# Optimization experiments

Hardware: AMD Instinct MI355X
Metric: run time of the kernel (lower is better)

## Reference

```python
import jax, jax.numpy as jnp
import numpy as np

N = 4096      # atoms
K = 5         # atoms gathered per cell (top_k in put_atoms_in_cells)
M = 8         # neighbors kept per atom
NBR = 26      # neighbor cells per cell (9+9+8)

def _grid():
    # get_cells: box [-10,10) step 1 Angstrom -> 20^3 = 8000 cells
    g = jnp.arange(-10.0, 10.0, 1.0)
    X = jnp.stack(jnp.meshgrid(g, g, g))       # (3,20,20,20), tf.meshgrid default 'xy'
    return jnp.transpose(X).reshape(-1, 3)      # (8000,3)

def _sqdist(a, b):
    # ||a_i - b_j||^2 via expansion; avoids (A,B,3) intermediate
    return (jnp.sum(a * a, 1)[:, None] + jnp.sum(b * b, 1)[None, :] - 2.0 * (a @ b.T))

def _neighbor_list(coords):
    cells = _grid()                              # (n_cells, 3)
    # put_atoms_in_cells: tf.nn.top_k(norm, k) -> k LARGEST norms (faithful to source)
    d_ca = _sqdist(cells, coords)                # (n_cells, N)
    _, atoms_in_cells = jax.lax.top_k(d_ca, K)   # (n_cells, K)
    # get_cells_for_atoms: top_k(-norm, 1) -> closest cell per atom
    d_ac = _sqdist(coords, cells)                # (N, n_cells)
    cells_for_atoms = jnp.argmin(d_ac, axis=1)   # (N,)
    # compute_neighbor_cells: top_k(norm, 26) (faithful to source)
    d_cc = _sqdist(cells, cells)                 # (n_cells, n_cells)
    _, nbr_cells = jax.lax.top_k(d_cc, NBR)      # (n_cells, 26)
    nbr_cells_atom = nbr_cells[cells_for_atoms]  # (N, 26)
    nbr_inds = atoms_in_cells[nbr_cells_atom]    # (N, 26, K)
    nbr_coords = coords[nbr_inds]                # (N, 26, K, 3)
    dists = jnp.sum((coords[:, None, None, :] - nbr_coords) ** 2, axis=-1)
    dists = dists.reshape(N, NBR * K)            # (N, 130)
    _, locs = jax.lax.top_k(dists, M)            # top_k(dists, M) as in source
    flat = nbr_inds.reshape(N, NBR * K)
    return jnp.take_along_axis(flat, locs, axis=1)   # (N, M) atom indices

def _energy(coords, vdw, weights, nrot, nbr):
    # d_ij = r_ij - R_i - R_j
    diff = coords[:, None, :] - coords[nbr]      # (N, M, 3)
    r = jnp.sqrt(jnp.sum(diff * diff, axis=-1) + 1e-12)
    d = r - vdw[:, None] - vdw[nbr]
    g1 = jnp.exp(-(d / 0.5) ** 2)
    g2 = jnp.exp(-((d - 3.0) / 2.0) ** 2)
    rep = jnp.where(d < 0.0, d * d, 0.0)
    hyd = jnp.where(d < 0.5, 1.0, jnp.where(d < 1.5, 1.5 - d, 0.0))
    hb = jnp.where(d < -0.7, 1.0, jnp.where(d < 0.0, -d / 0.7, 0.0))
    hval = (weights[0] * g1 + weights[1] * g2 + weights[2] * rep
            + weights[3] * hyd + weights[4] * hb)
    f = jnp.where(d < 8.0, hval, 0.0)            # cutoff at 8 Angstrom
    c = jnp.sum(f)
    return c / (1.0 + weights[5] * nrot[0])      # g(c, Nrot)

def setup_inputs() -> dict:
    key = jax.random.key(0)
    k1, k2, k3 = jax.random.split(key, 3)
    coords = jax.random.uniform(k1, (N, 3), jnp.float32, -10.0, 10.0)
    vdw = jax.random.uniform(k2, (N,), jnp.float32, 1.0, 2.0)
    weights = 0.3 * jax.random.normal(k3, (6,), jnp.float32)
    nrot = 8.0 * jnp.ones((1,), jnp.float32)
    return {"coords": coords, "vdw": vdw, "weights": weights, "nrot": nrot}

def reference(coords, vdw, weights, nrot):
    nbr = _neighbor_list(coords)
    return _energy(coords, vdw, weights, nrot, nbr)
```

## Files before the change

kernel.cpp:

```cpp
#include <hip/hip_runtime.h>
#include <stdint.h>

#define NATOMS 4096
#define NCELLS 8000
#define KTOP 5
#define MNBR 8
#define NBRC 26
#define HBINS 217
#define LSTMAX 512

__device__ __forceinline__ unsigned long long umax64(unsigned long long a, unsigned long long b) {
    return a > b ? a : b;
}
__device__ __forceinline__ unsigned long long umin64(unsigned long long a, unsigned long long b) {
    return a < b ? a : b;
}

__device__ __forceinline__ void cell_coords_i(int m, int& x, int& y, int& z) {
    int a = m / 400;
    int r = m - a * 400;
    int b = r / 20;
    int c = r - b * 20;
    x = b - 10; y = c - 10; z = a - 10;
}

__global__ __launch_bounds__(256) void k1_cells_nbr(const float* __restrict__ coords,
                                                    int* __restrict__ cellsForAtoms,
                                                    int* __restrict__ nbrTable,
                                                    int* __restrict__ neededFlag) {
    const int atom = blockIdx.x;
    const int t = threadIdx.x;
    const int lane = t & 63;

    __shared__ int sCi;
    __shared__ uint32_t h[HBINS];
    __shared__ int lst[LSTMAX];
    __shared__ int sV, cnt;

    if (t < HBINS) h[t] = 0;
    if (t == 0) cnt = 0;

    if (t < 64) {
        float ax = coords[atom * 3], ay = coords[atom * 3 + 1], az = coords[atom * 3 + 2];
        float sa = __fadd_rn(__fadd_rn(__fmul_rn(ax, ax), __fmul_rn(ay, ay)), __fmul_rn(az, az));

        int fx = (int)floorf(ax), fy = (int)floorf(ay), fz = (int)floorf(az);
        int vx = min(9, max(-10, fx - 1 + (lane & 3)));
        int vy = min(9, max(-10, fy - 1 + ((lane >> 2) & 3)));
        int vz = min(9, max(-10, fz - 1 + (lane >> 4)));
        int m = (vz + 10) * 400 + (vx + 10) * 20 + (vy + 10);

        float cx = (float)vx, cy = (float)vy, cz = (float)vz;
        float scell = (float)(vx * vx + vy * vy + vz * vz);
        float dot = __fadd_rn(__fadd_rn(__fmul_rn(ax, cx), __fmul_rn(ay, cy)), __fmul_rn(az, cz));
        float val = __fsub_rn(__fadd_rn(sa, scell), __fmul_rn(2.0f, dot));
        unsigned long long key = ((unsigned long long)__float_as_uint(val) << 32) | (unsigned int)m;

        for (int off = 32; off > 0; off >>= 1)
            key = umin64(key, (unsigned long long)__shfl_xor((long long)key, off));
        if (lane == 0) {
            int c = (int)(key & 0xFFFFFFFFull);
            cellsForAtoms[atom] = c;
            sCi = c;
        }
    }
    __syncthreads();

    const int ci = sCi;
    int xi, yi, zi;
    cell_coords_i(ci, xi, yi, zi);
    const int Lx = max(xi + 10, 9 - xi);
    const int Ly = max(yi + 10, 9 - yi);
    const int Lz = max(zi + 10, 9 - zi);

    int lo;
    {
        int px[3] = { Lx * Lx, (Lx - 1) * (Lx - 1), (Lx - 2) * (Lx - 2) };
        int py[3] = { Ly * Ly, (Ly - 1) * (Ly - 1), (Ly - 2) * (Ly - 2) };
        int pz[3] = { Lz * Lz, (Lz - 1) * (Lz - 1), (Lz - 2) * (Lz - 2) };
        int m1 = 0x7FFFFFFF, m2 = 0x7FFFFFFF;
#pragma unroll
        for (int a = 0; a < 3; ++a)
#pragma unroll
            for (int b = 0; b < 3; ++b)
#pragma unroll
                for (int c = 0; c < 3; ++c) {
                    int s = px[a] + py[b] + pz[c];
                    if (s < m1) { m2 = m1; m1 = s; }
                    else if (s < m2) m2 = s;
                }
        lo = m2;
    }

#pragma unroll
    for (int col = 0; col < 2; ++col) {
        int p = t + 256 * col;
        if (p < 400) {
            int bb = p / 20, cc = p - bb * 20;
            int dxv = xi - (bb - 10), dyv = yi - (cc - 10);
            int Dbc = dxv * dxv + dyv * dyv;
            int R = lo - Dbc;
            int aLoEnd = 19, aHiStart = 20;
            if (R > 0) {
                int t0 = (int)ceilf(sqrtf((float)R));
                if ((t0 - 1) * (t0 - 1) >= R) --t0;
                if (t0 * t0 < R) ++t0;
                aLoEnd = min(19, zi + 10 - t0);
                aHiStart = max(0, zi + 10 + t0);
            }
            for (int a = 0; a <= aLoEnd; ++a) {
                int dzv = zi - (a - 10);
                atomicAdd(&h[Dbc + dzv * dzv - lo], 1u);
            }
            for (int a = aHiStart; a < 20; ++a) {
                int dzv = zi - (a - 10);
                atomicAdd(&h[Dbc + dzv * dzv - lo], 1u);
            }
        }
    }
    __syncthreads();

    if (t < 64) {
        int c4[4];
        int cnt4 = 0;
#pragma unroll
        for (int k = 0; k < 4; ++k) {
            int b = (HBINS - 1) - (t * 4 + k);
            c4[k] = (b >= 0) ? (int)h[b] : 0;
            cnt4 += c4[k];
        }
        int incl = cnt4;
        for (int off = 1; off < 64; off <<= 1) {
            int v = __shfl_up(incl, off);
            if (lane >= off) incl += v;
        }
        int P = incl - cnt4;
        if (P < NBRC && incl >= NBRC) {
            int run = P;
#pragma unroll
            for (int k = 0; k < 4; ++k) {
                run += c4[k];
                if (run >= NBRC) { sV = lo + (HBINS - 1) - (t * 4 + k); break; }
            }
        }
    }
    __syncthreads();
    const int V = sV;

#pragma unroll
    for (int col = 0; col < 2; ++col) {
        int p = t + 256 * col;
        if (p < 400) {
            int bb = p / 20, cc = p - bb * 20;
            int dxv = xi - (bb - 10), dyv = yi - (cc - 10);
            int Dbc = dxv * dxv + dyv * dyv;
            int R = V - Dbc;
            int aLoEnd = 19, aHiStart = 20;
            if (R > 0) {
                int t0 = (int)ceilf(sqrtf((float)R));
                if ((t0 - 1) * (t0 - 1) >= R) --t0;
                if (t0 * t0 < R) ++t0;
                aLoEnd = min(19, zi + 10 - t0);
                aHiStart = max(0, zi + 10 + t0);
            }
            for (int a = 0; a <= aLoEnd; ++a) {
                int dzv = zi - (a - 10);
                int d = Dbc + dzv * dzv;
                int j = a * 400 + p;
                int q = atomicAdd(&cnt, 1);
                if (q < LSTMAX) lst[q] = (d << 13) | (8191 - j);
            }
            for (int a = aHiStart; a < 20; ++a) {
                int dzv = zi - (a - 10);
                int d = Dbc + dzv * dzv;
                int j = a * 400 + p;
                int q = atomicAdd(&cnt, 1);
                if (q < LSTMAX) lst[q] = (d << 13) | (8191 - j);
            }
        }
    }
    __syncthreads();

    int n = min(cnt, LSTMAX);
    if (t < 64) {
        for (int base = 0; base < n; base += 64) {
            int idx = base + t;
            int key = (idx < n) ? lst[idx] : -1;
            int rank = 0;
            for (int m = 0; m < n; ++m) rank += (lst[m] > key) ? 1 : 0;
            if (idx < n && rank < NBRC) {
                int j = 8191 - (key & 8191);
                nbrTable[ci * NBRC + rank] = j;
                neededFlag[j] = 1;
            }
        }
    }
}

__global__ __launch_bounds__(256) void k2_atoms(const float* __restrict__ coords,
                                                const int* __restrict__ neededFlag,
                                                int* __restrict__ atomsInCells) {
    const int i = blockIdx.x;
    if (neededFlag[i] != 1) return;
    __shared__ unsigned long long redB[4];
    const int t = threadIdx.x;
    const int lane = t & 63, wv = t >> 6;

    int xi_, yi_, zi_;
    cell_coords_i(i, xi_, yi_, zi_);
    const float cx = (float)xi_, cy = (float)yi_, cz = (float)zi_;
    const float scell = (float)(xi_ * xi_ + yi_ * yi_ + zi_ * zi_);

    unsigned long long keys[16];
#pragma unroll
    for (int s = 0; s < 16; ++s) {
        int j = t + 256 * s;
        float ax = coords[j * 3], ay = coords[j * 3 + 1], az = coords[j * 3 + 2];
        float sa = __fadd_rn(__fadd_rn(__fmul_rn(ax, ax), __fmul_rn(ay, ay)), __fmul_rn(az, az));
        float dot = __fadd_rn(__fadd_rn(__fmul_rn(cx, ax), __fmul_rn(cy, ay)), __fmul_rn(cz, az));
        float val = __fsub_rn(__fadd_rn(scell, sa), __fmul_rn(2.0f, dot));
        keys[s] = ((unsigned long long)__float_as_uint(val) << 32) | (unsigned int)(4095 - j);
    }

    for (int r = 0; r < KTOP; ++r) {
        unsigned long long best = 0ull;
#pragma unroll
        for (int s = 0; s < 16; ++s) best = umax64(best, keys[s]);
        for (int off = 32; off > 0; off >>= 1)
            best = umax64(best, (unsigned long long)__shfl_xor((long long)best, off));
        if (lane == 0) redB[wv] = best;
        __syncthreads();
        unsigned long long wbest = umax64(umax64(redB[0], redB[1]), umax64(redB[2], redB[3]));
        if (t == 0) atomsInCells[i * KTOP + r] = 4095 - (int)(wbest & 0xFFFFFFFFull);
#pragma unroll
        for (int s = 0; s < 16; ++s) if (keys[s] == wbest) keys[s] = 0ull;
        __syncthreads();
    }
}

__global__ __launch_bounds__(256) void k3_energy(const float* __restrict__ coords,
                                                 const float* __restrict__ vdw,
                                                 const float* __restrict__ weights,
                                                 const int* __restrict__ nbrTable,
                                                 const int* __restrict__ atomsInCells,
                                                 const int* __restrict__ cellsForAtoms,
                                                 float* __restrict__ partials) {
    const int wid = threadIdx.x >> 6;
    const int lane = threadIdx.x & 63;
    const int i = blockIdx.x * 4 + wid;

    const float xi = coords[i * 3], yi = coords[i * 3 + 1], zi = coords[i * 3 + 2];
    const int ci = cellsForAtoms[i];

    int cand[3];
    unsigned long long keys[3];
#pragma unroll
    for (int s = 0; s < 3; ++s) {
        int p = lane + 64 * s;
        cand[s] = -1;
        keys[s] = 0ull;
        if (p < NBRC * KTOP) {
            int cellSlot = p / KTOP;
            int atomSlot = p - cellSlot * KTOP;
            int nc = nbrTable[ci * NBRC + cellSlot];
            int j = atomsInCells[nc * KTOP + atomSlot];
            cand[s] = j;
            float dx = __fsub_rn(xi, coords[j * 3]);
            float dy = __fsub_rn(yi, coords[j * 3 + 1]);
            float dz = __fsub_rn(zi, coords[j * 3 + 2]);
            float dist = __fadd_rn(__fadd_rn(__fmul_rn(dx, dx), __fmul_rn(dy, dy)), __fmul_rn(dz, dz));
            keys[s] = ((unsigned long long)__float_as_uint(dist) << 8) | (unsigned int)(255 - p);
        }
    }

    const float w0 = weights[0], w1 = weights[1], w2 = weights[2];
    const float w3 = weights[3], w4 = weights[4];
    const float vi = vdw[i];

    float esum = 0.0f;
    for (int r = 0; r < MNBR; ++r) {
        unsigned long long best = umax64(umax64(keys[0], keys[1]), keys[2]);
        for (int off = 32; off > 0; off >>= 1)
            best = umax64(best, (unsigned long long)__shfl_xor((long long)best, off));

        int p = 255 - (int)(best & 0xFFull);
        int slot = p >> 6;
        int owner = p & 63;
        int jsel = (slot == 0) ? cand[0] : (slot == 1) ? cand[1] : cand[2];
        int j = __shfl(jsel, owner);
        float dist = __uint_as_float((unsigned int)(best >> 8));

#pragma unroll
        for (int s = 0; s < 3; ++s) if (keys[s] == best) keys[s] = 0ull;

        float rr = __fsqrt_rn(__fadd_rn(dist, 1e-12f));
        float d = __fsub_rn(__fsub_rn(rr, vi), vdw[j]);
        float t1 = __fdiv_rn(d, 0.5f);
        float g1 = expf(-__fmul_rn(t1, t1));
        float t2 = __fdiv_rn(__fsub_rn(d, 3.0f), 2.0f);
        float g2 = expf(-__fmul_rn(t2, t2));
        float rep = (d < 0.0f) ? __fmul_rn(d, d) : 0.0f;
        float hyd = (d < 0.5f) ? 1.0f : ((d < 1.5f) ? __fsub_rn(1.5f, d) : 0.0f);
        float hb = (d < -0.7f) ? 1.0f : ((d < 0.0f) ? __fdiv_rn(-d, 0.7f) : 0.0f);
        float hval = __fadd_rn(__fadd_rn(__fadd_rn(__fadd_rn(
                         __fmul_rn(w0, g1), __fmul_rn(w1, g2)),
                         __fmul_rn(w2, rep)), __fmul_rn(w3, hyd)), __fmul_rn(w4, hb));
        float f = (d < 8.0f) ? hval : 0.0f;
        esum = __fadd_rn(esum, f);
    }
    if (lane == 0) partials[i] = esum;
}

__global__ __launch_bounds__(256) void k4_reduce(const float* __restrict__ partials,
                                                 const float* __restrict__ weights,
                                                 const float* __restrict__ nrot,
                                                 float* __restrict__ out) {
    __shared__ float red[256];
    const int t = threadIdx.x;
    float s = 0.0f;
    for (int k = 0; k < NATOMS / 256; ++k) s = __fadd_rn(s, partials[t + 256 * k]);
    red[t] = s;
    __syncthreads();
    for (int off = 128; off > 0; off >>= 1) {
        if (t < off) red[t] = __fadd_rn(red[t], red[t + off]);
        __syncthreads();
    }
    if (t == 0) out[0] = __fdiv_rn(red[0], __fadd_rn(1.0f, __fmul_rn(weights[5], nrot[0])));
}

extern "C" void kernel_launch(void* const* d_in, const int* in_sizes, int n_in,
                              void* d_out, int out_size, void* d_ws, size_t ws_size,
                              hipStream_t stream) {
    const float* coords  = (const float*)d_in[0];
    const float* vdw     = (const float*)d_in[1];
    const float* weights = (const float*)d_in[2];
    const float* nrot    = (const float*)d_in[3];
    float* out = (float*)d_out;

    int* nbrTable      = (int*)d_ws;
    int* atomsInCells  = nbrTable + NCELLS * NBRC;
    int* cellsForAtoms = atomsInCells + NCELLS * KTOP;
    int* neededFlag    = cellsForAtoms + NATOMS;
    float* partials    = (float*)(neededFlag + NCELLS);

    k1_cells_nbr<<<NATOMS, 256, 0, stream>>>(coords, cellsForAtoms, nbrTable, neededFlag);
    k2_atoms<<<NCELLS, 256, 0, stream>>>(coords, neededFlag, atomsInCells);
    k3_energy<<<NATOMS / 4, 256, 0, stream>>>(coords, vdw, weights, nbrTable,
                                              atomsInCells, cellsForAtoms, partials);
    k4_reduce<<<1, 256, 0, stream>>>(partials, weights, nrot, out);
}
```

Measured before the change: 42.56 us.

## Simplify farthest-cell enumeration, per-wave top-k merge, and cache atom norms

The 27-way threshold search in the neighbor-cell kernel becomes a closed-form lower bound, and the sqrt-based z-range computation becomes early-break scans from both ends of the z column. Ranking of the candidate list now spreads over all 256 threads instead of one wave. In the atom-gather kernel, each wave keeps its own top-5 with no per-round block barriers, and a final rank-merge of 20 candidates picks the block's top-5. Atom squared norms computed in the first kernel are reused in the second to avoid recomputation. The risks are subtle correctness changes in the lower bound and in ties during the wave merge.

Result: faster. 39.49 us (-7.2%).

```diff
diff --git a/kernel.cpp b/kernel.cpp
--- a/kernel.cpp
+++ b/kernel.cpp
@@ -6,7 +6,7 @@
 #define KTOP 5
 #define MNBR 8
 #define NBRC 26
-#define HBINS 217
+#define HBINS 184
 #define LSTMAX 512
 
 __device__ __forceinline__ unsigned long long umax64(unsigned long long a, unsigned long long b) {
@@ -26,6 +26,7 @@
 
 __global__ __launch_bounds__(256) void k1_cells_nbr(const float* __restrict__ coords,
                                                     int* __restrict__ cellsForAtoms,
+                                                    float* __restrict__ sumsq,
                                                     int* __restrict__ nbrTable,
                                                     int* __restrict__ neededFlag) {
     const int atom = blockIdx.x;
@@ -61,6 +62,7 @@
         if (lane == 0) {
             int c = (int)(key & 0xFFFFFFFFull);
             cellsForAtoms[atom] = c;
+            sumsq[atom] = sa;
             sCi = c;
         }
     }
@@ -72,25 +74,9 @@
     const int Lx = max(xi + 10, 9 - xi);
     const int Ly = max(yi + 10, 9 - yi);
     const int Lz = max(zi + 10, 9 - zi);
-
-    int lo;
-    {
-        int px[3] = { Lx * Lx, (Lx - 1) * (Lx - 1), (Lx - 2) * (Lx - 2) };
-        int py[3] = { Ly * Ly, (Ly - 1) * (Ly - 1), (Ly - 2) * (Ly - 2) };
-        int pz[3] = { Lz * Lz, (Lz - 1) * (Lz - 1), (Lz - 2) * (Lz - 2) };
-        int m1 = 0x7FFFFFFF, m2 = 0x7FFFFFFF;
-#pragma unroll
-        for (int a = 0; a < 3; ++a)
-#pragma unroll
-            for (int b = 0; b < 3; ++b)
-#pragma unroll
-                for (int c = 0; c < 3; ++c) {
-                    int s = px[a] + py[b] + pz[c];
-                    if (s < m1) { m2 = m1; m1 = s; }
-                    else if (s < m2) m2 = s;
-                }
-        lo = m2;
-    }
+    const int lo = (Lx - 2) * (Lx - 2) + (Ly - 2) * (Ly - 2) + (Lz - 2) * (Lz - 2)
+                 + 2 * min(Lx, min(Ly, Lz)) - 3;
+    const int A0 = zi + 10;
 
 #pragma unroll
     for (int col = 0; col < 2; ++col) {
@@ -99,22 +85,20 @@
             int bb = p / 20, cc = p - bb * 20;
             int dxv = xi - (bb - 10), dyv = yi - (cc - 10);
             int Dbc = dxv * dxv + dyv * dyv;
-            int R = lo - Dbc;
-            int aLoEnd = 19, aHiStart = 20;
-            if (R > 0) {
-                int t0 = (int)ceilf(sqrtf((float)R));
-                if ((t0 - 1) * (t0 - 1) >= R) --t0;
-                if (t0 * t0 < R) ++t0;
-                aLoEnd = min(19, zi + 10 - t0);
-                aHiStart = max(0, zi + 10 + t0);
-            }
-            for (int a = 0; a <= aLoEnd; ++a) {
-                int dzv = zi - (a - 10);
-                atomicAdd(&h[Dbc + dzv * dzv - lo], 1u);
-            }
-            for (int a = aHiStart; a < 20; ++a) {
-                int dzv = zi - (a - 10);
-                atomicAdd(&h[Dbc + dzv * dzv - lo], 1u);
+            int a = 0;
+            for (; a < 20; ++a) {
+                int dz = A0 - a;
+                int d = Dbc + dz * dz;
+                if (d < lo) break;
+                atomicAdd(&h[d - lo], 1u);
+            }
+            if (a < 20) {
+                for (int a2 = 19; a2 >= a; --a2) {
+                    int dz = A0 - a2;
+                    int d = Dbc + dz * dz;
+                    if (d < lo) break;
+                    atomicAdd(&h[d - lo], 1u);
+                }
             }
         }
     }
@@ -154,55 +138,47 @@
             int bb = p / 20, cc = p - bb * 20;
             int dxv = xi - (bb - 10), dyv = yi - (cc - 10);
             int Dbc = dxv * dxv + dyv * dyv;
-            int R = V - Dbc;
-            int aLoEnd = 19, aHiStart = 20;
-            if (R > 0) {
-                int t0 = (int)ceilf(sqrtf((float)R));
-                if ((t0 - 1) * (t0 - 1) >= R) --t0;
-                if (t0 * t0 < R) ++t0;
-                aLoEnd = min(19, zi + 10 - t0);
-                aHiStart = max(0, zi + 10 + t0);
-            }
-            for (int a = 0; a <= aLoEnd; ++a) {
-                int dzv = zi - (a - 10);
-                int d = Dbc + dzv * dzv;
-                int j = a * 400 + p;
+            int a = 0;
+            for (; a < 20; ++a) {
+                int dz = A0 - a;
+                int d = Dbc + dz * dz;
+                if (d < V) break;
                 int q = atomicAdd(&cnt, 1);
-                if (q < LSTMAX) lst[q] = (d << 13) | (8191 - j);
-            }
-            for (int a = aHiStart; a < 20; ++a) {
-                int dzv = zi - (a - 10);
-                int d = Dbc + dzv * dzv;
-                int j = a * 400 + p;
-                int q = atomicAdd(&cnt, 1);
-                if (q < LSTMAX) lst[q] = (d << 13) | (8191 - j);
+                if (q < LSTMAX) lst[q] = (d << 13) | (8191 - (a * 400 + p));
+            }
+            if (a < 20) {
+                for (int a2 = 19; a2 >= a; --a2) {
+                    int dz = A0 - a2;
+                    int d = Dbc + dz * dz;
+                    if (d < V) break;
+                    int q = atomicAdd(&cnt, 1);
+                    if (q < LSTMAX) lst[q] = (d << 13) | (8191 - (a2 * 400 + p));
+                }
             }
         }
     }
     __syncthreads();
 
     int n = min(cnt, LSTMAX);
-    if (t < 64) {
-        for (int base = 0; base < n; base += 64) {
-            int idx = base + t;
-            int key = (idx < n) ? lst[idx] : -1;
-            int rank = 0;
-            for (int m = 0; m < n; ++m) rank += (lst[m] > key) ? 1 : 0;
-            if (idx < n && rank < NBRC) {
-                int j = 8191 - (key & 8191);
-                nbrTable[ci * NBRC + rank] = j;
-                neededFlag[j] = 1;
-            }
+    for (int idx = t; idx < n; idx += 256) {
+        int key = lst[idx];
+        int rank = 0;
+        for (int m = 0; m < n; ++m) rank += (lst[m] > key) ? 1 : 0;
+        if (rank < NBRC) {
+            int j = 8191 - (key & 8191);
+            nbrTable[ci * NBRC + rank] = j;
+            neededFlag[j] = 1;
         }
     }
 }
 
 __global__ __launch_bounds__(256) void k2_atoms(const float* __restrict__ coords,
+                                                const float* __restrict__ sumsq,
                                                 const int* __restrict__ neededFlag,
                                                 int* __restrict__ atomsInCells) {
     const int i = blockIdx.x;
     if (neededFlag[i] != 1) return;
-    __shared__ unsigned long long redB[4];
+    __shared__ unsigned long long wl[4 * KTOP];
     const int t = threadIdx.x;
     const int lane = t & 63, wv = t >> 6;
 
@@ -216,7 +192,7 @@
     for (int s = 0; s < 16; ++s) {
         int j = t + 256 * s;
         float ax = coords[j * 3], ay = coords[j * 3 + 1], az = coords[j * 3 + 2];
-        float sa = __fadd_rn(__fadd_rn(__fmul_rn(ax, ax), __fmul_rn(ay, ay)), __fmul_rn(az, az));
+        float sa = sumsq[j];
         float dot = __fadd_rn(__fadd_rn(__fmul_rn(cx, ax), __fmul_rn(cy, ay)), __fmul_rn(cz, az));
         float val = __fsub_rn(__fadd_rn(scell, sa), __fmul_rn(2.0f, dot));
         keys[s] = ((unsigned long long)__float_as_uint(val) << 32) | (unsigned int)(4095 - j);
@@ -228,13 +204,17 @@
         for (int s = 0; s < 16; ++s) best = umax64(best, keys[s]);
         for (int off = 32; off > 0; off >>= 1)
             best = umax64(best, (unsigned long long)__shfl_xor((long long)best, off));
-        if (lane == 0) redB[wv] = best;
-        __syncthreads();
-        unsigned long long wbest = umax64(umax64(redB[0], redB[1]), umax64(redB[2], redB[3]));
-        if (t == 0) atomsInCells[i * KTOP + r] = 4095 - (int)(wbest & 0xFFFFFFFFull);
-#pragma unroll
-        for (int s = 0; s < 16; ++s) if (keys[s] == wbest) keys[s] = 0ull;
-        __syncthreads();
+        if (lane == 0) wl[wv * KTOP + r] = best;
+#pragma unroll
+        for (int s = 0; s < 16; ++s) if (keys[s] == best) keys[s] = 0ull;
+    }
+    __syncthreads();
+
+    if (t < 4 * KTOP) {
+        unsigned long long key = wl[t];
+        int rank = 0;
+        for (int m = 0; m < 4 * KTOP; ++m) rank += (wl[m] > key) ? 1 : 0;
+        if (rank < KTOP) atomsInCells[i * KTOP + rank] = 4095 - (int)(key & 0xFFFFFFFFull);
     }
 }
 
@@ -342,9 +322,11 @@
     int* cellsForAtoms = atomsInCells + NCELLS * KTOP;
     int* neededFlag    = cellsForAtoms + NATOMS;
     float* partials    = (float*)(neededFlag + NCELLS);
-
-    k1_cells_nbr<<<NATOMS, 256, 0, stream>>>(coords, cellsForAtoms, nbrTable, neededFlag);
-    k2_atoms<<<NCELLS, 256, 0, stream>>>(coords, neededFlag, atomsInCells);
+    float* sumsq       = partials + NATOMS;
+
+    k1_cells_nbr<<<NATOMS, 256, 0, stream>>>(coords, cellsForAtoms, sumsq,
+                                             nbrTable, neededFlag);
+    k2_atoms<<<NCELLS, 256, 0, stream>>>(coords, sumsq, neededFlag, atomsInCells);
     k3_energy<<<NATOMS / 4, 256, 0, stream>>>(coords, vdw, weights, nbrTable,
                                               atomsInCells, cellsForAtoms, partials);
     k4_reduce<<<1, 256, 0, stream>>>(partials, weights, nrot, out);
```
